# Optimization experiments

Hardware: AMD Instinct MI355X
Metric: run time of the kernel (lower is better)

Reference implementation:

```python
import jax, jax.numpy as jnp
import numpy as np

N_E = 1024
E_DIM = 256
BETA = 0.25
EMA_LAMBDA = 0.99

def setup_inputs() -> dict:
    key = jax.random.key(0)
    k1, k2 = jax.random.split(key)
    z = jax.random.normal(k1, (32, 2048, E_DIM), dtype=jnp.float32)
    # torch init: uniform(-1/n_e, 1/n_e)
    embedding = jax.random.uniform(k2, (N_E, E_DIM), dtype=jnp.float32,
                                   minval=-1.0 / N_E, maxval=1.0 / N_E)
    N_t = jnp.zeros((N_E,), dtype=jnp.float32)
    m_t = jnp.zeros((N_E, E_DIM), dtype=jnp.float32)
    return {"z": z, "embedding": embedding, "N_t": N_t, "m_t": m_t}

def reference(z, embedding, N_t, m_t):
    zf = z.reshape(-1, E_DIM)  # [N, e_dim]
    # squared L2 distances: ||z||^2 + ||e||^2 - 2 z e^T  -> [N, n_e]
    d = (jnp.sum(zf * zf, axis=1, keepdims=True)
         + jnp.sum(embedding * embedding, axis=1)
         - 2.0 * jnp.matmul(zf, embedding.T))
    idx = jnp.argmin(d, axis=1)  # [N] int

    # EMA statistics (torch does a python loop over unique indices; this is the
    # vectorized equivalent: only codes that were selected get updated).
    counts = jax.ops.segment_sum(jnp.ones_like(idx, dtype=jnp.float32), idx, num_segments=N_E)
    sums = jax.ops.segment_sum(zf, idx, num_segments=N_E)  # [n_e, e_dim]
    selected = counts > 0
    N_t_new = jnp.where(selected, N_t * EMA_LAMBDA + counts * (1.0 - EMA_LAMBDA), N_t)
    m_t_new = jnp.where(selected[:, None], m_t * EMA_LAMBDA + sums * (1.0 - EMA_LAMBDA), m_t)

    z_q = embedding[idx].reshape(z.shape)
    loss = BETA * jnp.mean((jax.lax.stop_gradient(z_q) - z) ** 2)
    z_q_st = z + jax.lax.stop_gradient(z_q - z)  # straight-through

    # perplexity from code usage histogram (== mean of one-hot encodings)
    e_mean = counts / idx.shape[0]
    perplexity = jnp.exp(-jnp.sum(e_mean * jnp.log(e_mean + 1e-10)))
    return (loss, z_q_st, idx, perplexity, N_t_new, m_t_new)
```

## Files before the change

kernel.cpp:

```cpp
#include <hip/hip_runtime.h>
#include <math.h>

#define N_ROWS  65536
#define EDIM    256
#define NE      1024
#define BETA    0.25f
#define LAMBDA  0.99f

#define MARGIN  8e-3f
#define QCAP    8192


#define O_ZQ   1
#define O_IDX  16777217
#define O_PERP 16842753
#define O_NT   16842754
#define O_MT   16843778

typedef __attribute__((ext_vector_type(8))) short short8;
typedef __attribute__((ext_vector_type(4))) float f32x4;

__device__ __forceinline__ unsigned short f2bf(float f) {
    unsigned u = __float_as_uint(f);
    return (unsigned short)((u + 0x7fffu + ((u >> 16) & 1u)) >> 16);
}

__global__ __launch_bounds__(64) void prep_b_kernel(const float* __restrict__ emb,
                                                    unsigned* __restrict__ bfrag_u32,
                                                    float* __restrict__ loss_acc,
                                                    int* __restrict__ cnt) {
    int j = blockIdx.x;
    int l = threadIdx.x;
    float4 v = ((const float4*)(emb + (size_t)j * EDIM))[l];
    unsigned lo = (unsigned)f2bf(v.x) | ((unsigned)f2bf(v.y) << 16);
    unsigned hi = (unsigned)f2bf(v.z) | ((unsigned)f2bf(v.w) << 16);
    int base = ((((j >> 4) * 8 + (l >> 3)) * 64) + ((l >> 1) & 3) * 16 + (j & 15)) * 4
             + 2 * (l & 1);
    bfrag_u32[base]     = lo;
    bfrag_u32[base + 1] = hi;
    if (l == 0) cnt[j] = 0;
    if (j == 0 && l == 0) *loss_acc = 0.0f;
}

__global__ __launch_bounds__(256) void sq_kernel(const float* __restrict__ src,
                                                 float* __restrict__ dst) {
    const int tid = threadIdx.x;
    const int grp = tid >> 4;
    const int q   = tid & 15;
    const int row = blockIdx.x * 16 + grp;
    const int h = q >> 3, j = q & 7;
    const float* __restrict__ p = src + (size_t)row * EDIM + h * 128 + j;
    float acc = __fmul_rn(p[0], p[0]);
    #pragma unroll
    for (int t = 1; t < 16; ++t) {
        float v = p[8 * t];
        acc = __fadd_rn(acc, __fmul_rn(v, v));
    }
    acc = __fadd_rn(acc, __shfl_xor(acc, 1));
    acc = __fadd_rn(acc, __shfl_xor(acc, 2));
    acc = __fadd_rn(acc, __shfl_xor(acc, 4));
    acc = __fadd_rn(acc, __shfl_xor(acc, 8));
    if (q == 0) dst[row] = acc;
}

__global__ __launch_bounds__(256) void prep_z_kernel(const float* __restrict__ z,
                                                     float* __restrict__ zsq) {
    __shared__ __align__(16) float a_lds[16 * EDIM];
    const int tid = threadIdx.x;
    const int row0 = blockIdx.x * 16;
    {
        const float4* __restrict__ src = (const float4*)(z + (size_t)row0 * EDIM);
        float4* dst = (float4*)a_lds;
        #pragma unroll
        for (int i = 0; i < 4; ++i) dst[tid + 256 * i] = src[tid + 256 * i];
    }
    __syncthreads();
    const int row = tid >> 4, q = tid & 15, h = q >> 3, j = q & 7;
    const float* p = a_lds + row * EDIM + h * 128 + j;
    float acc = __fmul_rn(p[0], p[0]);
    #pragma unroll
    for (int t = 1; t < 16; ++t) {
        float v = p[8 * t];
        acc = __fadd_rn(acc, __fmul_rn(v, v));
    }
    acc = __fadd_rn(acc, __shfl_xor(acc, 1));
    acc = __fadd_rn(acc, __shfl_xor(acc, 2));
    acc = __fadd_rn(acc, __shfl_xor(acc, 4));
    acc = __fadd_rn(acc, __shfl_xor(acc, 8));
    if (q == 0) zsq[row0 + row] = acc;
}

__global__ __launch_bounds__(512, 2) void argmin_kernel(const float* __restrict__ z,
                                                        const float* __restrict__ emb,
                                                        const float4* __restrict__ bsrc,
                                                        const float* __restrict__ e_sq,
                                                        const float* __restrict__ zsq,
                                                        int* __restrict__ idx_out,
                                                        float* __restrict__ out_zq,
                                                        float* __restrict__ out_idx,
                                                        float* __restrict__ loss_acc) {
    __shared__ __align__(16) float4 Bs[2048];
    __shared__ unsigned long long best_s[256];
    __shared__ int queue[QCAP];
    __shared__ int qcnt;
    __shared__ int idx_s[256];
    __shared__ float lred[8];

    const int tid  = threadIdx.x;
    const int wid  = tid >> 6, lane = tid & 63;
    const int l15  = lane & 15, lg = lane >> 4;
    const int row0 = blockIdx.x * 256;
    const int rbase = row0 + wid * 32;

    if (tid < 256) best_s[tid] = ~0ull;
    if (tid == 0) qcnt = 0;

    float4 st[4];
    #pragma unroll
    for (int i = 0; i < 4; ++i) st[i] = bsrc[tid + 512 * i];

    short8 a[2][8];
    #pragma unroll
    for (int rt = 0; rt < 2; ++rt) {
        #pragma unroll
        for (int ks = 0; ks < 8; ++ks) {
            const float* zp = z + (size_t)(rbase + rt * 16 + l15) * EDIM + ks * 32 + lg * 8;
            float4 f0 = *(const float4*)zp;
            float4 f1 = *(const float4*)(zp + 4);
            union { short8 s; unsigned short u[8]; } pk;
            pk.u[0] = f2bf(f0.x); pk.u[1] = f2bf(f0.y); pk.u[2] = f2bf(f0.z); pk.u[3] = f2bf(f0.w);
            pk.u[4] = f2bf(f1.x); pk.u[5] = f2bf(f1.y); pk.u[6] = f2bf(f1.z); pk.u[7] = f2bf(f1.w);
            a[rt][ks] = pk.s;
        }
    }

    float rm[2][4];
    #pragma unroll
    for (int rt = 0; rt < 2; ++rt)
        #pragma unroll
        for (int r = 0; r < 4; ++r) rm[rt][r] = 1e30f;

    __syncthreads();

    for (int ch = 0; ch < 16; ++ch) {
        const int cb = ch * 64;
        #pragma unroll
        for (int i = 0; i < 4; ++i) Bs[tid + 512 * i] = st[i];
        __syncthreads();
        if (ch < 15) {
            #pragma unroll
            for (int i = 0; i < 4; ++i) st[i] = bsrc[(ch + 1) * 2048 + tid + 512 * i];
        }

        float eqs[4];
        #pragma unroll
        for (int ct = 0; ct < 4; ++ct) eqs[ct] = e_sq[cb + ct * 16 + l15];

        f32x4 acc[2][4];
        #pragma unroll
        for (int rt = 0; rt < 2; ++rt)
            #pragma unroll
            for (int ct = 0; ct < 4; ++ct) acc[rt][ct] = (f32x4){0.f, 0.f, 0.f, 0.f};

        const short8* Bv = (const short8*)Bs;
        #pragma unroll
        for (int ks = 0; ks < 8; ++ks) {
            #pragma unroll
            for (int ct = 0; ct < 4; ++ct) {
                short8 b = Bv[(ct * 8 + ks) * 64 + lane];
                acc[0][ct] = __builtin_amdgcn_mfma_f32_16x16x32_bf16(a[0][ks], b, acc[0][ct], 0, 0, 0);
                acc[1][ct] = __builtin_amdgcn_mfma_f32_16x16x32_bf16(a[1][ks], b, acc[1][ct], 0, 0, 0);
            }
        }

        #pragma unroll
        for (int rt = 0; rt < 2; ++rt) {
            #pragma unroll
            for (int r = 0; r < 4; ++r) {
                float m = __fsub_rn(eqs[0], __fmul_rn(2.0f, acc[rt][0][r]));
                #pragma unroll
                for (int ct = 1; ct < 4; ++ct) {
                    float t = __fsub_rn(eqs[ct], __fmul_rn(2.0f, acc[rt][ct][r]));
                    m = fminf(m, t);
                }
                m = fminf(m, __shfl_xor(m, 1));
                m = fminf(m, __shfl_xor(m, 2));
                m = fminf(m, __shfl_xor(m, 4));
                m = fminf(m, __shfl_xor(m, 8));
                rm[rt][r] = fminf(rm[rt][r], m);
            }
        }

        #pragma unroll
        for (int rt = 0; rt < 2; ++rt) {
            #pragma unroll
            for (int ct = 0; ct < 4; ++ct) {
                #pragma unroll
                for (int r = 0; r < 4; ++r) {
                    float t = __fsub_rn(eqs[ct], __fmul_rn(2.0f, acc[rt][ct][r]));
                    if (t <= rm[rt][r] + MARGIN) {
                        int rl  = wid * 32 + rt * 16 + lg * 4 + r;
                        int col = cb + ct * 16 + l15;
                        int s = atomicAdd(&qcnt, 1);
                        if (s < QCAP) queue[s] = (rl << 10) | col;
                    }
                }
            }
        }
        __syncthreads();
    }

    __syncthreads();

    {
        int nq = qcnt; if (nq > QCAP) nq = QCAP;
        const int g = tid >> 3, q = tid & 7;
        for (int e = g; e < nq; e += 64) {
            int ent = queue[e];
            int rl = ent >> 10, col = ent & 1023;
            const float4* zr = (const float4*)(z + (size_t)(row0 + rl) * EDIM);
            const float4* er = (const float4*)(emb + (size_t)col * EDIM);
            float ae = 0.f;
            #pragma unroll
            for (int i = 0; i < 8; ++i) {
                float4 x = zr[q + 8 * i], y = er[q + 8 * i];
                ae = __fmaf_rn(x.x, y.x, ae);
                ae = __fmaf_rn(x.y, y.y, ae);
                ae = __fmaf_rn(x.z, y.z, ae);
                ae = __fmaf_rn(x.w, y.w, ae);
            }
            ae = __fadd_rn(ae, __shfl_xor(ae, 1));
            ae = __fadd_rn(ae, __shfl_xor(ae, 2));
            ae = __fadd_rn(ae, __shfl_xor(ae, 4));
            if (q == 0) {
                float d = __fsub_rn(__fadd_rn(zsq[row0 + rl], e_sq[col]), __fmul_rn(2.0f, ae));
                unsigned u = __float_as_uint(d);
                u = (u & 0x80000000u) ? ~u : (u | 0x80000000u);
                unsigned long long key = ((unsigned long long)u << 32) | (unsigned)col;
                atomicMin(&best_s[rl], key);
            }
        }
    }

    __syncthreads();
    if (tid < 256) {
        unsigned long long k = best_s[tid];
        int id = (int)(k & 0xffffffffull);
        idx_out[row0 + tid] = id;
        out_idx[row0 + tid] = (float)id;
        idx_s[tid] = id;
    }
    __syncthreads();

    const float4* e4 = (const float4*)emb;
    for (int i = 0; i < 32; ++i) {
        int flat = tid + i * 512;
        int r = flat >> 6, c4 = flat & 63;
        int id = idx_s[r];
        float4 e = e4[(size_t)id * 64 + c4];
        float* o = out_zq + (size_t)(row0 + r) * EDIM + c4 * 4;
        o[0] = e.x; o[1] = e.y; o[2] = e.z; o[3] = e.w;
    }

    float lp = 0.f;
    if (tid < 256) {
        unsigned m = (unsigned)(best_s[tid] >> 32);
        unsigned bits = (m & 0x80000000u) ? (m & 0x7fffffffu) : ~m;
        lp = __uint_as_float(bits);
    }
    #pragma unroll
    for (int m = 32; m; m >>= 1) lp += __shfl_down(lp, m);
    if (lane == 0) lred[wid] = lp;
    __syncthreads();
    if (tid == 0) {
        float s = lred[0] + lred[1] + lred[2] + lred[3]
                + lred[4] + lred[5] + lred[6] + lred[7];
        atomicAdd(loss_acc, s);
    }
}

__global__ __launch_bounds__(256) void hist_kernel(const int* __restrict__ idx,
                                                   int* __restrict__ cnt) {
    int i = blockIdx.x * 256 + threadIdx.x;
    atomicAdd(&cnt[idx[i]], 1);
}

__global__ __launch_bounds__(1024) void scan_kernel(const int* __restrict__ cnt,
                                                    const float* __restrict__ N_t,
                                                    float* __restrict__ outN,
                                                    float* __restrict__ counts_f,
                                                    int* __restrict__ offs,
                                                    int* __restrict__ cursor) {
    __shared__ int s[1024];
    const int tid = threadIdx.x;
    int c = cnt[tid];
    s[tid] = c;
    __syncthreads();
    for (int d = 1; d < 1024; d <<= 1) {
        int v = (tid >= d) ? s[tid - d] : 0;
        __syncthreads();
        s[tid] += v;
        __syncthreads();
    }
    int excl = s[tid] - c;
    offs[tid] = excl;
    cursor[tid] = excl;
    counts_f[tid] = (float)c;
    float Nold = N_t[tid];
    outN[tid] = (c > 0) ? Nold * LAMBDA + (float)c * (1.0f - LAMBDA) : Nold;
}

__global__ __launch_bounds__(256) void scatter_kernel(const int* __restrict__ idx,
                                                      int* __restrict__ cursor,
                                                      int* __restrict__ sorted) {
    int i = blockIdx.x * 256 + threadIdx.x;
    int p = atomicAdd(&cursor[idx[i]], 1);
    sorted[p] = i;
}

__global__ __launch_bounds__(256) void msum_kernel(const float* __restrict__ z,
                                                   const int* __restrict__ sorted,
                                                   const int* __restrict__ offs,
                                                   const int* __restrict__ cnt,
                                                   const float* __restrict__ m_t,
                                                   float* __restrict__ outM) {
    const int j = blockIdx.x;
    const int tid = threadIdx.x, w = tid >> 6, lane = tid & 63;
    const int n = cnt[j], start = offs[j];
    float4 acc = make_float4(0.f, 0.f, 0.f, 0.f);
    for (int e = w; e < n; e += 4) {
        float4 v = ((const float4*)(z + (size_t)sorted[start + e] * EDIM))[lane];
        acc.x += v.x; acc.y += v.y; acc.z += v.z; acc.w += v.w;
    }
    __shared__ float red[4 * 256];
    *(float4*)(red + w * 256 + lane * 4) = acc;
    __syncthreads();
    if (tid < 256) {
        float s = red[tid] + red[256 + tid] + red[512 + tid] + red[768 + tid];
        float mold = m_t[(size_t)j * EDIM + tid];
        outM[(size_t)j * EDIM + tid] = (n > 0) ? mold * LAMBDA + s * (1.0f - LAMBDA) : mold;
    }
}

__global__ __launch_bounds__(256) void final_kernel(const float* __restrict__ counts,
                                                    const float* __restrict__ loss_acc,
                                                    float* __restrict__ out_loss,
                                                    float* __restrict__ out_perp) {
    const int tid = threadIdx.x, w = tid >> 6, lane = tid & 63;
    float h = 0.f;
    for (int c = tid; c < NE; c += 256) {
        float em = counts[c] * (1.0f / (float)N_ROWS);
        h += em * logf(em + 1e-10f);
    }
    #pragma unroll
    for (int m = 32; m; m >>= 1) h += __shfl_down(h, m);
    __shared__ float red[4];
    if (lane == 0) red[w] = h;
    __syncthreads();
    if (tid == 0) {
        float H = red[0] + red[1] + red[2] + red[3];
        out_perp[0] = expf(-H);
        out_loss[0] = BETA * loss_acc[0] * (1.0f / (float)(N_ROWS * EDIM));
    }
}

extern "C" void kernel_launch(void* const* d_in, const int* in_sizes, int n_in,
                              void* d_out, int out_size, void* d_ws, size_t ws_size,
                              hipStream_t stream) {
    const float* z   = (const float*)d_in[0];
    const float* emb = (const float*)d_in[1];
    const float* N_t = (const float*)d_in[2];
    const float* m_t = (const float*)d_in[3];
    float* out = (float*)d_out;
    float* ws  = (float*)d_ws;

    float* loss_acc   = ws;
    float* e_sq       = ws + 64;
    float* zsq        = ws + 2048;
    unsigned* bfrag_u = (unsigned*)(ws + 67584);
    int*   sorted     = (int*)(ws + 198656);
    int*   idx1       = (int*)(ws + 264192);
    float* counts     = ws + 329728;
    int*   cnt_i      = (int*)(ws + 330752);
    int*   offs_i     = (int*)(ws + 331776);
    int*   cursor_i   = (int*)(ws + 332800);

    prep_b_kernel<<<NE, 64, 0, stream>>>(emb, bfrag_u, loss_acc, cnt_i);
    sq_kernel<<<NE / 16, 256, 0, stream>>>(emb, e_sq);
    prep_z_kernel<<<N_ROWS / 16, 256, 0, stream>>>(z, zsq);
    argmin_kernel<<<N_ROWS / 256, 512, 0, stream>>>(z, emb, (const float4*)bfrag_u,
                                                    e_sq, zsq, idx1,
                                                    out + O_ZQ, out + O_IDX, loss_acc);
    hist_kernel<<<N_ROWS / 256, 256, 0, stream>>>(idx1, cnt_i);
    scan_kernel<<<1, 1024, 0, stream>>>(cnt_i, N_t, out + O_NT, counts, offs_i, cursor_i);
    scatter_kernel<<<N_ROWS / 256, 256, 0, stream>>>(idx1, cursor_i, sorted);
    msum_kernel<<<NE, 256, 0, stream>>>(z, sorted, offs_i, cnt_i, m_t, out + O_MT);
    final_kernel<<<1, 256, 0, stream>>>(counts, loss_acc, out, out + O_PERP);
}
```

Baseline: 366.2 us.

## Fuse z-norm and histogram into argmin kernel, shrink blocks, filter stale candidates

Computes row squared norms of z inside the argmin kernel while loading and converting z, and drops the separate prep_z kernel along with its global zsq buffer. The histogram atomics also move into argmin, removing hist_kernel. Blocks shrink to 256 threads and 128 rows with three blocks per CU. Queue entries now carry the approximate distance, so candidates beyond the final running minimum plus margin are skipped before the exact fp32 recheck. The risk is that the row norm is now summed in a different order than the reference, and the smaller queue capacity could overflow and drop candidates.

```diff
diff --git a/kernel.cpp b/kernel.cpp
--- a/kernel.cpp
+++ b/kernel.cpp
@@ -8,7 +8,7 @@
 #define LAMBDA  0.99f
 
 #define MARGIN  8e-3f
-#define QCAP    8192
+#define QCAP    2048
 
 
 #define O_ZQ   1
@@ -63,75 +63,56 @@
     if (q == 0) dst[row] = acc;
 }
 
-__global__ __launch_bounds__(256) void prep_z_kernel(const float* __restrict__ z,
-                                                     float* __restrict__ zsq) {
-    __shared__ __align__(16) float a_lds[16 * EDIM];
-    const int tid = threadIdx.x;
-    const int row0 = blockIdx.x * 16;
-    {
-        const float4* __restrict__ src = (const float4*)(z + (size_t)row0 * EDIM);
-        float4* dst = (float4*)a_lds;
-        #pragma unroll
-        for (int i = 0; i < 4; ++i) dst[tid + 256 * i] = src[tid + 256 * i];
-    }
-    __syncthreads();
-    const int row = tid >> 4, q = tid & 15, h = q >> 3, j = q & 7;
-    const float* p = a_lds + row * EDIM + h * 128 + j;
-    float acc = __fmul_rn(p[0], p[0]);
-    #pragma unroll
-    for (int t = 1; t < 16; ++t) {
-        float v = p[8 * t];
-        acc = __fadd_rn(acc, __fmul_rn(v, v));
-    }
-    acc = __fadd_rn(acc, __shfl_xor(acc, 1));
-    acc = __fadd_rn(acc, __shfl_xor(acc, 2));
-    acc = __fadd_rn(acc, __shfl_xor(acc, 4));
-    acc = __fadd_rn(acc, __shfl_xor(acc, 8));
-    if (q == 0) zsq[row0 + row] = acc;
-}
-
-__global__ __launch_bounds__(512, 2) void argmin_kernel(const float* __restrict__ z,
+__global__ __launch_bounds__(256, 3) void argmin_kernel(const float* __restrict__ z,
                                                         const float* __restrict__ emb,
                                                         const float4* __restrict__ bsrc,
                                                         const float* __restrict__ e_sq,
-                                                        const float* __restrict__ zsq,
                                                         int* __restrict__ idx_out,
                                                         float* __restrict__ out_zq,
                                                         float* __restrict__ out_idx,
-                                                        float* __restrict__ loss_acc) {
+                                                        float* __restrict__ loss_acc,
+                                                        int* __restrict__ cnt) {
     __shared__ __align__(16) float4 Bs[2048];
-    __shared__ unsigned long long best_s[256];
-    __shared__ int queue[QCAP];
+    __shared__ uint2 queue[QCAP];
+    __shared__ unsigned long long best_s[128];
+    __shared__ int   idx_s[128];
+    __shared__ float zsq_s[128];
+    __shared__ float rmF_s[128];
+    __shared__ float lred[4];
     __shared__ int qcnt;
-    __shared__ int idx_s[256];
-    __shared__ float lred[8];
 
     const int tid  = threadIdx.x;
     const int wid  = tid >> 6, lane = tid & 63;
     const int l15  = lane & 15, lg = lane >> 4;
-    const int row0 = blockIdx.x * 256;
+    const int row0 = blockIdx.x * 128;
     const int rbase = row0 + wid * 32;
 
-    if (tid < 256) best_s[tid] = ~0ull;
+    if (tid < 128) best_s[tid] = ~0ull;
     if (tid == 0) qcnt = 0;
 
-    float4 st[4];
-    #pragma unroll
-    for (int i = 0; i < 4; ++i) st[i] = bsrc[tid + 512 * i];
+    float4 st[8];
+    #pragma unroll
+    for (int i = 0; i < 8; ++i) st[i] = bsrc[tid + 256 * i];
 
     short8 a[2][8];
     #pragma unroll
     for (int rt = 0; rt < 2; ++rt) {
+        float zs = 0.f;
         #pragma unroll
         for (int ks = 0; ks < 8; ++ks) {
             const float* zp = z + (size_t)(rbase + rt * 16 + l15) * EDIM + ks * 32 + lg * 8;
             float4 f0 = *(const float4*)zp;
             float4 f1 = *(const float4*)(zp + 4);
+            zs += f0.x * f0.x + f0.y * f0.y + f0.z * f0.z + f0.w * f0.w
+                + f1.x * f1.x + f1.y * f1.y + f1.z * f1.z + f1.w * f1.w;
             union { short8 s; unsigned short u[8]; } pk;
             pk.u[0] = f2bf(f0.x); pk.u[1] = f2bf(f0.y); pk.u[2] = f2bf(f0.z); pk.u[3] = f2bf(f0.w);
             pk.u[4] = f2bf(f1.x); pk.u[5] = f2bf(f1.y); pk.u[6] = f2bf(f1.z); pk.u[7] = f2bf(f1.w);
             a[rt][ks] = pk.s;
         }
+        zs += __shfl_xor(zs, 16);
+        zs += __shfl_xor(zs, 32);
+        if (lg == 0) zsq_s[wid * 32 + rt * 16 + l15] = zs;
     }
 
     float rm[2][4];
@@ -145,11 +126,11 @@
     for (int ch = 0; ch < 16; ++ch) {
         const int cb = ch * 64;
         #pragma unroll
-        for (int i = 0; i < 4; ++i) Bs[tid + 512 * i] = st[i];
+        for (int i = 0; i < 8; ++i) Bs[tid + 256 * i] = st[i];
         __syncthreads();
         if (ch < 15) {
             #pragma unroll
-            for (int i = 0; i < 4; ++i) st[i] = bsrc[(ch + 1) * 2048 + tid + 512 * i];
+            for (int i = 0; i < 8; ++i) st[i] = bsrc[(ch + 1) * 2048 + tid + 256 * i];
         }
 
         float eqs[4];
@@ -202,7 +183,8 @@
                         int rl  = wid * 32 + rt * 16 + lg * 4 + r;
                         int col = cb + ct * 16 + l15;
                         int s = atomicAdd(&qcnt, 1);
-                        if (s < QCAP) queue[s] = (rl << 10) | col;
+                        if (s < QCAP) queue[s] = make_uint2((rl << 10) | col,
+                                                            __float_as_uint(t));
                     }
                 }
             }
@@ -210,14 +192,20 @@
         __syncthreads();
     }
 
+    #pragma unroll
+    for (int rt = 0; rt < 2; ++rt)
+        #pragma unroll
+        for (int r = 0; r < 4; ++r)
+            if (l15 == 0) rmF_s[wid * 32 + rt * 16 + lg * 4 + r] = rm[rt][r];
     __syncthreads();
 
     {
         int nq = qcnt; if (nq > QCAP) nq = QCAP;
         const int g = tid >> 3, q = tid & 7;
-        for (int e = g; e < nq; e += 64) {
-            int ent = queue[e];
-            int rl = ent >> 10, col = ent & 1023;
+        for (int e = g; e < nq; e += 32) {
+            uint2 ent = queue[e];
+            int rl = ent.x >> 10, col = ent.x & 1023;
+            if (__uint_as_float(ent.y) > rmF_s[rl] + MARGIN) continue;
             const float4* zr = (const float4*)(z + (size_t)(row0 + rl) * EDIM);
             const float4* er = (const float4*)(emb + (size_t)col * EDIM);
             float ae = 0.f;
@@ -233,7 +221,7 @@
             ae = __fadd_rn(ae, __shfl_xor(ae, 2));
             ae = __fadd_rn(ae, __shfl_xor(ae, 4));
             if (q == 0) {
-                float d = __fsub_rn(__fadd_rn(zsq[row0 + rl], e_sq[col]), __fmul_rn(2.0f, ae));
+                float d = __fsub_rn(__fadd_rn(zsq_s[rl], e_sq[col]), __fmul_rn(2.0f, ae));
                 unsigned u = __float_as_uint(d);
                 u = (u & 0x80000000u) ? ~u : (u | 0x80000000u);
                 unsigned long long key = ((unsigned long long)u << 32) | (unsigned)col;
@@ -243,18 +231,19 @@
     }
 
     __syncthreads();
-    if (tid < 256) {
+    if (tid < 128) {
         unsigned long long k = best_s[tid];
         int id = (int)(k & 0xffffffffull);
         idx_out[row0 + tid] = id;
         out_idx[row0 + tid] = (float)id;
         idx_s[tid] = id;
+        atomicAdd(&cnt[id], 1);
     }
     __syncthreads();
 
     const float4* e4 = (const float4*)emb;
     for (int i = 0; i < 32; ++i) {
-        int flat = tid + i * 512;
+        int flat = tid + i * 256;
         int r = flat >> 6, c4 = flat & 63;
         int id = idx_s[r];
         float4 e = e4[(size_t)id * 64 + c4];
@@ -263,7 +252,7 @@
     }
 
     float lp = 0.f;
-    if (tid < 256) {
+    if (tid < 128) {
         unsigned m = (unsigned)(best_s[tid] >> 32);
         unsigned bits = (m & 0x80000000u) ? (m & 0x7fffffffu) : ~m;
         lp = __uint_as_float(bits);
@@ -273,16 +262,9 @@
     if (lane == 0) lred[wid] = lp;
     __syncthreads();
     if (tid == 0) {
-        float s = lred[0] + lred[1] + lred[2] + lred[3]
-                + lred[4] + lred[5] + lred[6] + lred[7];
+        float s = lred[0] + lred[1] + lred[2] + lred[3];
         atomicAdd(loss_acc, s);
     }
-}
-
-__global__ __launch_bounds__(256) void hist_kernel(const int* __restrict__ idx,
-                                                   int* __restrict__ cnt) {
-    int i = blockIdx.x * 256 + threadIdx.x;
-    atomicAdd(&cnt[idx[i]], 1);
 }
 
 __global__ __launch_bounds__(1024) void scan_kernel(const int* __restrict__ cnt,
@@ -376,7 +358,6 @@
 
     float* loss_acc   = ws;
     float* e_sq       = ws + 64;
-    float* zsq        = ws + 2048;
     unsigned* bfrag_u = (unsigned*)(ws + 67584);
     int*   sorted     = (int*)(ws + 198656);
     int*   idx1       = (int*)(ws + 264192);
@@ -387,11 +368,9 @@
 
     prep_b_kernel<<<NE, 64, 0, stream>>>(emb, bfrag_u, loss_acc, cnt_i);
     sq_kernel<<<NE / 16, 256, 0, stream>>>(emb, e_sq);
-    prep_z_kernel<<<N_ROWS / 16, 256, 0, stream>>>(z, zsq);
-    argmin_kernel<<<N_ROWS / 256, 512, 0, stream>>>(z, emb, (const float4*)bfrag_u,
-                                                    e_sq, zsq, idx1,
-                                                    out + O_ZQ, out + O_IDX, loss_acc);
-    hist_kernel<<<N_ROWS / 256, 256, 0, stream>>>(idx1, cnt_i);
+    argmin_kernel<<<N_ROWS / 128, 256, 0, stream>>>(z, emb, (const float4*)bfrag_u,
+                                                    e_sq, idx1,
+                                                    out + O_ZQ, out + O_IDX, loss_acc, cnt_i);
     scan_kernel<<<1, 1024, 0, stream>>>(cnt_i, N_t, out + O_NT, counts, offs_i, cursor_i);
     scatter_kernel<<<N_ROWS / 256, 256, 0, stream>>>(idx1, cursor_i, sorted);
     msum_kernel<<<NE, 256, 0, stream>>>(z, sorted, offs_i, cnt_i, m_t, out + O_MT);
```

New measurement: 342.6 us. -6.5%, faster.
